# Optimization experiments

Measured on AMD Instinct MI355X. Metric: run time of the kernel, lower is better.

The kernel has to match this reference:

```python
import jax, jax.numpy as jnp
import numpy as np

N, E = 50000, 800000
S, V, RBF_DIM = 128, 16, 16
RBF_DMAX = 20.0
MSG_NORM = 10.0
EPS = 1e-8
DVH_M = V + 1            # message GVP: dim_vectors_in = V + 1 (edge direction appended), dim_h = max(17,16) = 17
FIN_M = S + RBF_DIM      # message GVP scalar input = node scalars + rbf(dist)
DVH_U = 2 * V            # update GVP: dim_vectors_in = 2V (node + aggregated), dim_h = 32
FIN_U = 2 * S


def _rbf(D):
    # [E] -> [E, RBF_DIM], matches torch _rbf with D_min=0, D_max=20, D_count=16
    D_mu = jnp.linspace(0.0, RBF_DMAX, RBF_DIM)
    D_sigma = RBF_DMAX / RBF_DIM
    return jnp.exp(-(((D[:, None] - D_mu[None, :]) / D_sigma) ** 2))


def _gvp(s, v, Wh, Wu, Wf, bf, Wg, bg):
    # s: [n, F_in], v: [n, V_in, 3]; faithful to GVP.forward with sigmoid vector gating
    Vh = jnp.einsum('nvc,vh->nhc', v, Wh)          # [n, H, 3]
    Vu = jnp.einsum('nhc,ho->noc', Vh, Wu)         # [n, V_out, 3]
    sh = jnp.sqrt(jnp.clip(jnp.sum(Vh * Vh, -1), EPS))  # _norm_no_nan
    feats_out = jax.nn.silu(jnp.concatenate([s, sh], -1) @ Wf + bf)
    gate = jax.nn.sigmoid(feats_out @ Wg + bg)[..., None]
    return feats_out, gate * Vu


def _gvp_layernorm(s, v, gamma, beta):
    mu = jnp.mean(s, -1, keepdims=True)
    var = jnp.mean((s - mu) ** 2, -1, keepdims=True)
    s_out = (s - mu) / jnp.sqrt(var + 1e-5) * gamma + beta
    vn = jnp.clip(jnp.sum(v * v, -1, keepdims=True), EPS)        # [N, V, 1]
    vn = jnp.sqrt(jnp.mean(vn, -2, keepdims=True) + 1e-5) + 1e-5  # [N, 1, 1]
    return s_out, v / vn


def setup_inputs() -> dict:
    key = jax.random.key(0)
    ks = jax.random.split(key, 14)
    rn = lambda k, shp, sc: (jax.random.normal(k, shp, dtype=jnp.float32) * sc)
    inp = {
        's': rn(ks[0], (N, S), 1.0),
        'v': rn(ks[1], (N, V, 3), 1.0),
        'x': rn(ks[2], (N, 3), 5.0),
        # message GVP params
        'Wh_m': rn(ks[3], (DVH_M, DVH_M), 1.0 / np.sqrt(DVH_M)),
        'Wu_m': rn(ks[4], (DVH_M, V), 1.0 / np.sqrt(DVH_M)),
        'Wf_m': rn(ks[5], (DVH_M + FIN_M, S), 1.0 / np.sqrt(DVH_M + FIN_M)),
        'bf_m': jnp.zeros((S,), jnp.float32),
        'Wg_m': rn(ks[6], (S, V), 1.0 / np.sqrt(S)),
        'bg_m': jnp.zeros((V,), jnp.float32),
        # update GVP params
        'Wh_u': rn(ks[7], (DVH_U, DVH_U), 1.0 / np.sqrt(DVH_U)),
        'Wu_u': rn(ks[8], (DVH_U, V), 1.0 / np.sqrt(DVH_U)),
        'Wf_u': rn(ks[9], (DVH_U + FIN_U, S), 1.0 / np.sqrt(DVH_U + FIN_U)),
        'bf_u': jnp.zeros((S,), jnp.float32),
        'Wg_u': rn(ks[10], (S, V), 1.0 / np.sqrt(S)),
        'bg_u': jnp.zeros((V,), jnp.float32),
        # layernorm
        'ln_g': jnp.ones((S,), jnp.float32),
        'ln_b': jnp.zeros((S,), jnp.float32),
        'edge_index': jax.random.randint(ks[11], (2, E), 0, N),
    }
    return inp


def reference(s, v, x, Wh_m, Wu_m, Wf_m, bf_m, Wg_m, bg_m,
              Wh_u, Wu_u, Wf_u, bf_u, Wg_u, bg_u, ln_g, ln_b, edge_index):
    src, dst = edge_index[0], edge_index[1]
    # gather + geometric edge features
    dx = x[dst] - x[src]                                   # [E, 3]
    dist = jnp.sqrt(jnp.clip(jnp.sum(dx * dx, -1), EPS))    # [E]
    unit = dx / dist[:, None]
    v_in = jnp.concatenate([v[src], unit[:, None, :]], 1)   # [E, V+1, 3]
    s_in = jnp.concatenate([s[src], _rbf(dist)], -1)        # [E, S+RBF]
    # message GVP
    ms, mv = _gvp(s_in, v_in, Wh_m, Wu_m, Wf_m, bf_m, Wg_m, bg_m)
    # scatter-reduce + message norm
    agg_s = jax.ops.segment_sum(ms, dst, num_segments=N) / MSG_NORM   # [N, S]
    agg_v = jax.ops.segment_sum(mv, dst, num_segments=N) / MSG_NORM   # [N, V, 3]
    # update GVP on concatenated node + aggregated messages
    us, uv = _gvp(jnp.concatenate([s, agg_s], -1), jnp.concatenate([v, agg_v], 1),
                  Wh_u, Wu_u, Wf_u, bf_u, Wg_u, bg_u)
    # residual + GVPLayerNorm
    return _gvp_layernorm(s + us, v + uv, ln_g, ln_b)
```

## Files before the change

### kernel.cpp

```cpp
#include <hip/hip_runtime.h>
#include <hip/hip_bf16.h>
#include <math.h>

#define N_NODES 50000
#define E_EDGES 800000
#define S_DIM 128
#define V_DIM 16
#define HM 17
#define KM 161
#define HU 32
#define KU 288

#define EB 32
#define LDA 164
#define NB 32
#define LDA2 292

__device__ __forceinline__ float bf2f(unsigned short u) {
    union { unsigned int i; float f; } w; w.i = ((unsigned int)u) << 16; return w.f;
}
__device__ __forceinline__ unsigned short f2bf(float f) {
    union { float f; unsigned int i; } w; w.f = f;
    unsigned int x = w.i;
    x += 0x7fff + ((x >> 16) & 1);
    return (unsigned short)(x >> 16);
}
__device__ __forceinline__ float silu_f(float x) { return x / (1.f + __expf(-x)); }
__device__ __forceinline__ float sigm_f(float x) { return 1.f / (1.f + __expf(-x)); }
__device__ __forceinline__ float ldf(const void* p, int i, int m) {
    if (m) return ((const float*)p)[i];
    return bf2f(((const unsigned short*)p)[i]);
}

__global__ void detect_kernel(const unsigned short* __restrict__ s_us,
                              int* __restrict__ flag) {
    int t = threadIdx.x;
    int huge = 0;
    for (int k = 0; k < 16; ++k) {
        unsigned short u = s_us[2 * (t + 64 * k)];
        int e = (u >> 7) & 0xFF;
        if (e > 140) huge = 1;
    }
    if (huge) atomicOr(flag, 1);
}

__global__ void hist_kernel(const int* __restrict__ ei, int* __restrict__ cnt) {
    int i = blockIdx.x * 256 + threadIdx.x;
    if (i < E_EDGES) atomicAdd(&cnt[ei[E_EDGES + i]], 1);
}

__global__ void scan_kernel(int* __restrict__ cnt) {
    __shared__ int buf[1024];
    __shared__ int base_s;
    const int t = threadIdx.x;
    if (t == 0) base_s = 0;
    __syncthreads();
    for (int c0 = 0; c0 < N_NODES; c0 += 1024) {
        int i = c0 + t;
        int v = (i < N_NODES) ? cnt[i] : 0;
        buf[t] = v;
        __syncthreads();
        for (int off = 1; off < 1024; off <<= 1) {
            int tmp = (t >= off) ? buf[t - off] : 0;
            __syncthreads();
            buf[t] += tmp;
            __syncthreads();
        }
        int base = base_s;
        if (i < N_NODES) cnt[i] = base + buf[t] - v;
        __syncthreads();
        if (t == 0) base_s = base + buf[1023];
        __syncthreads();
    }
}

__global__ void scatter_kernel(const int* __restrict__ ei,
                               int* __restrict__ cnt,
                               int* __restrict__ perm) {
    int i = blockIdx.x * 256 + threadIdx.x;
    if (i < E_EDGES) {
        int d = ei[E_EDGES + i];
        int p = atomicAdd(&cnt[d], 1);
        perm[p] = i;
    }
}

__global__ __launch_bounds__(256, 4) void edge_kernel(
    const void* sP, const void* vP, const void* xP,
    const void* WhP, const void* WuP, const void* WfP,
    const void* bfP, const void* WgP, const void* bgP,
    const int* __restrict__ ei,
    const int* __restrict__ perm,
    const int* __restrict__ flagp,
    float* __restrict__ agg_s,
    float* __restrict__ agg_v)
{
    __shared__ float A[EB * LDA];
    __shared__ float Bs[2048];
    __shared__ float WhWu[HM * 16];
    __shared__ float gates[EB * 16];
    __shared__ int srcb[EB], dstb[EB];

    const int t = threadIdx.x;
    const int e0 = blockIdx.x * EB;
    const int m = flagp[0];

    if (t < EB) {
        int eid = perm[e0 + t];
        srcb[t] = ei[eid];
        dstb[t] = ei[E_EDGES + eid];
    }
    if (m) {
        const float* Wh = (const float*)WhP;
        const float* Wu = (const float*)WuP;
        for (int i = t; i < HM * HM; i += 256) gates[i] = Wh[i];
        for (int i = t; i < HM * 16; i += 256) Bs[1664 + i] = Wu[i];
    } else {
        const unsigned short* Wh = (const unsigned short*)WhP;
        const unsigned short* Wu = (const unsigned short*)WuP;
        for (int i = t; i < HM * HM; i += 256) gates[i] = bf2f(Wh[i]);
        for (int i = t; i < HM * 16; i += 256) Bs[1664 + i] = bf2f(Wu[i]);
    }
    __syncthreads();

    for (int idx = t; idx < HM * 16; idx += 256) {
        int vv = idx / 16, o = idx % 16;
        float acc = 0.f;
        for (int h = 0; h < HM; ++h)
            acc += gates[vv * HM + h] * Bs[1664 + h * 16 + o];
        WhWu[idx] = acc;
    }
    {
        int tj = t & 31, te = t >> 5;
        if (m) {
            const float* sF = (const float*)sP;
            for (int r = 0; r < 4; ++r) {
                int e = te + 8 * r;
                float4 u = *(const float4*)(sF + (size_t)srcb[e] * S_DIM + tj * 4);
                float* a = &A[e * LDA + tj * 4];
                a[0] = u.x; a[1] = u.y; a[2] = u.z; a[3] = u.w;
            }
        } else {
            const unsigned short* sU = (const unsigned short*)sP;
            for (int r = 0; r < 4; ++r) {
                int e = te + 8 * r;
                ushort4 u = *(const ushort4*)(sU + (size_t)srcb[e] * S_DIM + tj * 4);
                float* a = &A[e * LDA + tj * 4];
                a[0] = bf2f(u.x); a[1] = bf2f(u.y); a[2] = bf2f(u.z); a[3] = bf2f(u.w);
            }
        }
    }
    if (t < 128) {
        int e = t >> 2, q = t & 3;
        int src = srcb[e];
        float* vin = &Bs[e * 52 + q * 12];
        if (m) {
            const float* vp = (const float*)vP + (size_t)src * 48 + q * 12;
            for (int i = 0; i < 3; ++i) {
                float4 u = *(const float4*)(vp + i * 4);
                vin[i * 4 + 0] = u.x; vin[i * 4 + 1] = u.y;
                vin[i * 4 + 2] = u.z; vin[i * 4 + 3] = u.w;
            }
        } else {
            const unsigned short* vp = (const unsigned short*)vP + (size_t)src * 48 + q * 12;
            for (int i = 0; i < 3; ++i) {
                ushort4 u = *(const ushort4*)(vp + i * 4);
                vin[i * 4 + 0] = bf2f(u.x); vin[i * 4 + 1] = bf2f(u.y);
                vin[i * 4 + 2] = bf2f(u.z); vin[i * 4 + 3] = bf2f(u.w);
            }
        }
        if (q == 0) {
            int dst = dstb[e];
            float dxc[3]; float d2 = 0.f;
            for (int c = 0; c < 3; ++c) {
                float xs = ldf(xP, src * 3 + c, m);
                float xd = ldf(xP, dst * 3 + c, m);
                dxc[c] = xd - xs; d2 += dxc[c] * dxc[c];
            }
            float dist = sqrtf(fmaxf(d2, 1e-8f));
            float inv = 1.f / dist;
            for (int c = 0; c < 3; ++c) Bs[e * 52 + 48 + c] = dxc[c] * inv;
            for (int k = 0; k < 16; ++k) {
                float mu = (20.f / 15.f) * (float)k;
                float z = (dist - mu) * (1.f / 1.25f);
                A[e * LDA + 128 + k] = __expf(-z * z);
            }
        }
    }
    __syncthreads();

    for (int idx = t; idx < EB * HM; idx += 256) {
        int e = idx / HM, h = idx % HM;
        const float* vin = &Bs[e * 52];
        float vh0 = 0.f, vh1 = 0.f, vh2 = 0.f;
        for (int vv = 0; vv < HM; ++vv) {
            float w = gates[vv * HM + h];
            vh0 += vin[vv * 3 + 0] * w;
            vh1 += vin[vv * 3 + 1] * w;
            vh2 += vin[vv * 3 + 2] * w;
        }
        A[e * LDA + 144 + h] = sqrtf(fmaxf(vh0 * vh0 + vh1 * vh1 + vh2 * vh2, 1e-8f));
    }
    float vureg[6];
    for (int r = 0; r < 6; ++r) {
        int idx = t + 256 * r;
        int e = idx / 48, oc = idx % 48, o = oc / 3, c = oc % 3;
        const float* vin = &Bs[e * 52];
        float acc = 0.f;
        for (int vv = 0; vv < HM; ++vv)
            acc += vin[vv * 3 + c] * WhWu[vv * 16 + o];
        vureg[r] = acc;
    }
    __syncthreads();

    const int tj = t & 15, te = t >> 4;
    const int eb = te * 2;
    float acc[2][8];
    #pragma unroll
    for (int i = 0; i < 2; ++i)
        #pragma unroll
        for (int j = 0; j < 8; ++j) acc[i][j] = 0.f;

    for (int kk = 0; kk < KM; kk += 16) {
        int kmax = min(16, KM - kk);
        if (m) {
            const float* WfF = (const float*)WfP;
            for (int idx = t; idx < kmax * 32; idx += 256) {
                int kt = idx >> 5, col4 = (idx & 31) * 4;
                float4 u = *(const float4*)(WfF + (size_t)(kk + kt) * 128 + col4);
                float* b = &Bs[kt * 128 + col4];
                b[0] = u.x; b[1] = u.y; b[2] = u.z; b[3] = u.w;
            }
        } else {
            const unsigned short* WfU = (const unsigned short*)WfP;
            for (int idx = t; idx < kmax * 32; idx += 256) {
                int kt = idx >> 5, col4 = (idx & 31) * 4;
                ushort4 u = *(const ushort4*)(WfU + (size_t)(kk + kt) * 128 + col4);
                float* b = &Bs[kt * 128 + col4];
                b[0] = bf2f(u.x); b[1] = bf2f(u.y); b[2] = bf2f(u.z); b[3] = bf2f(u.w);
            }
        }
        __syncthreads();
        for (int kt = 0; kt < kmax; ++kt) {
            float a0 = A[(eb + 0) * LDA + kk + kt];
            float a1 = A[(eb + 1) * LDA + kk + kt];
            const float* brow = &Bs[kt * 128 + tj];
            #pragma unroll
            for (int jj = 0; jj < 8; ++jj) {
                float b = brow[16 * jj];
                acc[0][jj] += a0 * b; acc[1][jj] += a1 * b;
            }
        }
        __syncthreads();
    }
    float breg[8];
    #pragma unroll
    for (int jj = 0; jj < 8; ++jj) breg[jj] = ldf(bfP, tj + 16 * jj, m);
    #pragma unroll
    for (int i = 0; i < 2; ++i) {
        float* aout = &A[(eb + i) * LDA];
        #pragma unroll
        for (int jj = 0; jj < 8; ++jj)
            aout[tj + 16 * jj] = silu_f(acc[i][jj] + breg[jj]);
    }
    __syncthreads();
    if (m) {
        const float* Wg = (const float*)WgP;
        for (int i = t; i < 2048; i += 256) Bs[i] = Wg[i];
    } else {
        const unsigned short* Wg = (const unsigned short*)WgP;
        for (int i = t; i < 2048; i += 256) Bs[i] = bf2f(Wg[i]);
    }
    __syncthreads();
    for (int r = 0; r < 2; ++r) {
        int idx = t + 256 * r;
        int e = idx / 16, o = idx % 16;
        const float* fe = &A[e * LDA];
        float g = ldf(bgP, o, m);
        for (int j = 0; j < S_DIM; ++j)
            g += fe[j] * Bs[j * 16 + o];
        gates[idx] = sigm_f(g);
    }
    __syncthreads();
    for (int r = 0; r < 6; ++r) {
        int idx = t + 256 * r;
        int e = idx / 48, oc = idx % 48, o = oc / 3;
        (void)oc;
        Bs[idx] = vureg[r] * gates[e * 16 + o];
    }
    __syncthreads();
    if (t < 176) {
        float run = 0.f;
        int cur = dstb[0];
        if (t < 128) {
            const int col = t;
            for (int e = 0; e < EB; ++e) {
                int d = dstb[e];
                if (d != cur) {
                    atomicAdd(&agg_s[(size_t)cur * S_DIM + col], run);
                    run = 0.f; cur = d;
                }
                run += A[e * LDA + col];
            }
            atomicAdd(&agg_s[(size_t)cur * S_DIM + col], run);
        } else {
            const int oc = t - 128;
            for (int e = 0; e < EB; ++e) {
                int d = dstb[e];
                if (d != cur) {
                    atomicAdd(&agg_v[(size_t)cur * 48 + oc], run);
                    run = 0.f; cur = d;
                }
                run += Bs[e * 48 + oc];
            }
            atomicAdd(&agg_v[(size_t)cur * 48 + oc], run);
        }
    }
}

__global__ __launch_bounds__(256) void node_kernel(
    const void* sP, const void* vP,
    const void* WhP, const void* WuP, const void* WfP,
    const void* bfP, const void* WgP, const void* bgP,
    const void* lngP, const void* lnbP,
    const int* __restrict__ flagp,
    const float* __restrict__ agg_s,
    const float* __restrict__ agg_v,
    void* outP)
{
    __shared__ float A2[NB * LDA2];
    __shared__ float Bs2[4096];
    __shared__ float WhWu2[HU * 16];
    __shared__ float gates2[NB * 16];
    __shared__ float WhS[HU * HU];
    __shared__ float mu_s[NB], rstd_s[NB], vn_s[NB];

    const int t = threadIdx.x;
    const int n0 = blockIdx.x * NB;
    const int m = flagp[0];

    if (m) {
        const float* Wh = (const float*)WhP;
        const float* Wu = (const float*)WuP;
        for (int i = t; i < HU * HU; i += 256) WhS[i] = Wh[i];
        for (int i = t; i < HU * 16; i += 256) gates2[i] = Wu[i];
    } else {
        const unsigned short* Wh = (const unsigned short*)WhP;
        const unsigned short* Wu = (const unsigned short*)WuP;
        for (int i = t; i < HU * HU; i += 256) WhS[i] = bf2f(Wh[i]);
        for (int i = t; i < HU * 16; i += 256) gates2[i] = bf2f(Wu[i]);
    }
    if (m) {
        const float* sF = (const float*)sP;
        for (int idx = t; idx < NB * 32; idx += 256) {
            int ni = idx >> 5, col4 = (idx & 31) * 4;
            int n = n0 + ni;
            float* a = &A2[ni * LDA2 + col4];
            if (n < N_NODES) {
                float4 u = *(const float4*)(sF + (size_t)n * 128 + col4);
                a[0] = u.x; a[1] = u.y; a[2] = u.z; a[3] = u.w;
            } else { a[0] = a[1] = a[2] = a[3] = 0.f; }
        }
    } else {
        const unsigned short* sU = (const unsigned short*)sP;
        for (int idx = t; idx < NB * 32; idx += 256) {
            int ni = idx >> 5, col4 = (idx & 31) * 4;
            int n = n0 + ni;
            float* a = &A2[ni * LDA2 + col4];
            if (n < N_NODES) {
                ushort4 u = *(const ushort4*)(sU + (size_t)n * 128 + col4);
                a[0] = bf2f(u.x); a[1] = bf2f(u.y); a[2] = bf2f(u.z); a[3] = bf2f(u.w);
            } else { a[0] = a[1] = a[2] = a[3] = 0.f; }
        }
    }
    for (int idx = t; idx < NB * 32; idx += 256) {
        int ni = idx >> 5, col4 = (idx & 31) * 4;
        int n = n0 + ni;
        float* a = &A2[ni * LDA2 + 128 + col4];
        if (n < N_NODES) {
            float4 u = *(const float4*)(agg_s + (size_t)n * 128 + col4);
            a[0] = u.x * 0.1f; a[1] = u.y * 0.1f; a[2] = u.z * 0.1f; a[3] = u.w * 0.1f;
        } else { a[0] = a[1] = a[2] = a[3] = 0.f; }
    }
    for (int idx = t; idx < NB * 96; idx += 256) {
        int ni = idx / 96, vc = idx % 96;
        int n = n0 + ni;
        float val = 0.f;
        if (n < N_NODES)
            val = (vc < 48) ? ldf(vP, n * 48 + vc, m)
                            : agg_v[(size_t)n * 48 + (vc - 48)] * 0.1f;
        Bs2[ni * 100 + vc] = val;
    }
    __syncthreads();
    for (int idx = t; idx < HU * 16; idx += 256) {
        int vv = idx / 16, o = idx % 16;
        float acc = 0.f;
        for (int h = 0; h < HU; ++h)
            acc += WhS[vv * HU + h] * gates2[h * 16 + o];
        WhWu2[idx] = acc;
// ... 69 lines not shown
        #pragma unroll
        for (int jj = 0; jj < 8; ++jj)
            aout[tj + 16 * jj] = silu_f(acc[i][jj] + breg[jj]);
    }
    __syncthreads();
    if (m) {
        const float* Wg = (const float*)WgP;
        for (int i = t; i < 2048; i += 256) Bs2[i] = Wg[i];
    } else {
        const unsigned short* Wg = (const unsigned short*)WgP;
        for (int i = t; i < 2048; i += 256) Bs2[i] = bf2f(Wg[i]);
    }
    __syncthreads();
    for (int r = 0; r < 2; ++r) {
        int idx = t + 256 * r;
        int ni = idx / 16, o = idx % 16;
        const float* fe = &A2[ni * LDA2 + 128];
        float g = ldf(bgP, o, m);
        for (int j = 0; j < 128; ++j)
            g += fe[j] * Bs2[j * 16 + o];
        gates2[idx] = sigm_f(g);
    }
    __syncthreads();
    for (int r = 0; r < 6; ++r) {
        int idx = t + 256 * r;
        int ni = idx / 48, oc = idx % 48, o = oc / 3;
        int n = n0 + ni;
        float vres = 0.f;
        if (n < N_NODES)
            vres = ldf(vP, n * 48 + oc, m) + vureg[r] * gates2[ni * 16 + o];
        Bs2[ni * 48 + oc] = vres;
    }
    __syncthreads();
    if (t < NB) {
        const float* arow = &A2[t * LDA2];
        float sum = 0.f, sumsq = 0.f;
        for (int j = 0; j < 128; ++j) {
            float xr = arow[j] + arow[128 + j];
            sum += xr; sumsq += xr * xr;
        }
        float mu = sum * (1.f / 128.f);
        float var = sumsq * (1.f / 128.f) - mu * mu;
        mu_s[t] = mu;
        rstd_s[t] = rsqrtf(fmaxf(var, 0.f) + 1e-5f);
        const float* vr = &Bs2[t * 48];
        float accv = 0.f;
        for (int o = 0; o < 16; ++o) {
            float mm = vr[o*3]*vr[o*3] + vr[o*3+1]*vr[o*3+1] + vr[o*3+2]*vr[o*3+2];
            accv += fmaxf(mm, 1e-8f);
        }
        vn_s[t] = sqrtf(accv * (1.f / 16.f) + 1e-5f) + 1e-5f;
    }
    __syncthreads();
    float* outF = (float*)outP;
    unsigned short* outU = (unsigned short*)outP;
    for (int idx = t; idx < NB * 128; idx += 256) {
        int ni = idx >> 7, j = idx & 127;
        int n = n0 + ni;
        if (n < N_NODES) {
            float xr = A2[ni * LDA2 + j] + A2[ni * LDA2 + 128 + j];
            float o = (xr - mu_s[ni]) * rstd_s[ni] * ldf(lngP, j, m) + ldf(lnbP, j, m);
            if (m) outF[(size_t)n * 128 + j] = o;
            else   outU[(size_t)n * 128 + j] = f2bf(o);
        }
    }
    for (int idx = t; idx < NB * 48; idx += 256) {
        int ni = idx / 48, oc = idx % 48;
        int n = n0 + ni;
        if (n < N_NODES) {
            float o = Bs2[ni * 48 + oc] / vn_s[ni];
            if (m) outF[(size_t)N_NODES * 128 + (size_t)n * 48 + oc] = o;
            else   outU[(size_t)N_NODES * 128 + (size_t)n * 48 + oc] = f2bf(o);
        }
    }
}

extern "C" void kernel_launch(void* const* d_in, const int* in_sizes, int n_in,
                              void* d_out, int out_size, void* d_ws, size_t ws_size,
                              hipStream_t stream) {
    const int* ei = (const int*)d_in[17];

    int* flag = (int*)d_ws;
    int* cnt = (int*)((char*)d_ws + 64);
    float* agg_s = (float*)((char*)d_ws + 64 + 200000);
    float* agg_v = agg_s + (size_t)N_NODES * 128;
    int* perm = (int*)(agg_v + (size_t)N_NODES * 48);

    hipMemsetAsync(d_ws, 0,
                   64 + 200000 + (size_t)N_NODES * (128 + 48) * sizeof(float),
                   stream);

    detect_kernel<<<1, 64, 0, stream>>>((const unsigned short*)d_in[0], flag);

    hist_kernel<<<(E_EDGES + 255) / 256, 256, 0, stream>>>(ei, cnt);
    scan_kernel<<<1, 1024, 0, stream>>>(cnt);
    scatter_kernel<<<(E_EDGES + 255) / 256, 256, 0, stream>>>(ei, cnt, perm);

    edge_kernel<<<E_EDGES / EB, 256, 0, stream>>>(
        d_in[0], d_in[1], d_in[2], d_in[3], d_in[4], d_in[5],
        d_in[6], d_in[7], d_in[8], ei, perm, flag, agg_s, agg_v);
    node_kernel<<<(N_NODES + NB - 1) / NB, 256, 0, stream>>>(
        d_in[0], d_in[1], d_in[9], d_in[10], d_in[11], d_in[12],
        d_in[13], d_in[14], d_in[15], d_in[16], flag,
        agg_s, agg_v, d_out);
}
```

Baseline: 2.534 ms.

## Precompute per-node linear terms of message GVP before edge gather

Adds a prep kernel that computes, once per source node, s·Wf[:128], the partial vector projection v·Wh and its Wu projection. The edge kernel then gathers these precomputed rows and adds only the edge-dependent terms (rbf, unit vector, vector norms) through a 33-row matmul. This moves the 128-wide scalar matmul from 800k edges to 50k nodes, at the cost of an extra kernel, extra workspace and gathering 128+51+48 floats per edge instead of 128+48 raw inputs.

```diff
diff --git a/kernel.cpp b/kernel.cpp
--- a/kernel.cpp
+++ b/kernel.cpp
@@ -12,9 +12,9 @@
 #define KU 288
 
 #define EB 32
-#define LDA 164
 #define NB 32
 #define LDA2 292
+#define LDF 132
 
 __device__ __forceinline__ float bf2f(unsigned short u) {
     union { unsigned int i; float f; } w; w.i = ((unsigned int)u) << 16; return w.f;
@@ -85,166 +85,113 @@
     }
 }
 
-__global__ __launch_bounds__(256, 4) void edge_kernel(
-    const void* sP, const void* vP, const void* xP,
+__global__ __launch_bounds__(256, 4) void prep_kernel(
+    const void* sP, const void* vP,
     const void* WhP, const void* WuP, const void* WfP,
-    const void* bfP, const void* WgP, const void* bgP,
-    const int* __restrict__ ei,
-    const int* __restrict__ perm,
     const int* __restrict__ flagp,
-    float* __restrict__ agg_s,
-    float* __restrict__ agg_v)
+    float* __restrict__ Pg, float* __restrict__ Qg, float* __restrict__ Rg,
+    float* __restrict__ whwu16)
 {
-    __shared__ float A[EB * LDA];
-    __shared__ float Bs[2048];
-    __shared__ float WhWu[HM * 16];
-    __shared__ float gates[EB * 16];
-    __shared__ int srcb[EB], dstb[EB];
+    __shared__ float sA[NB * 132];
+    __shared__ float Wfb[16 * 128];
+    __shared__ float vtile[NB * 48];
+    __shared__ float WhS[HM * HM];
+    __shared__ float WuS[HM * 16];
 
     const int t = threadIdx.x;
-    const int e0 = blockIdx.x * EB;
+    const int n0 = blockIdx.x * NB;
     const int m = flagp[0];
 
-    if (t < EB) {
-        int eid = perm[e0 + t];
-        srcb[t] = ei[eid];
-        dstb[t] = ei[E_EDGES + eid];
-    }
     if (m) {
         const float* Wh = (const float*)WhP;
         const float* Wu = (const float*)WuP;
-        for (int i = t; i < HM * HM; i += 256) gates[i] = Wh[i];
-        for (int i = t; i < HM * 16; i += 256) Bs[1664 + i] = Wu[i];
+        for (int i = t; i < HM * HM; i += 256) WhS[i] = Wh[i];
+        for (int i = t; i < HM * 16; i += 256) WuS[i] = Wu[i];
     } else {
         const unsigned short* Wh = (const unsigned short*)WhP;
         const unsigned short* Wu = (const unsigned short*)WuP;
-        for (int i = t; i < HM * HM; i += 256) gates[i] = bf2f(Wh[i]);
-        for (int i = t; i < HM * 16; i += 256) Bs[1664 + i] = bf2f(Wu[i]);
-    }
-    __syncthreads();
-
-    for (int idx = t; idx < HM * 16; idx += 256) {
-        int vv = idx / 16, o = idx % 16;
-        float acc = 0.f;
-        for (int h = 0; h < HM; ++h)
-            acc += gates[vv * HM + h] * Bs[1664 + h * 16 + o];
-        WhWu[idx] = acc;
-    }
-    {
-        int tj = t & 31, te = t >> 5;
-        if (m) {
-            const float* sF = (const float*)sP;
-            for (int r = 0; r < 4; ++r) {
-                int e = te + 8 * r;
-                float4 u = *(const float4*)(sF + (size_t)srcb[e] * S_DIM + tj * 4);
-                float* a = &A[e * LDA + tj * 4];
+        for (int i = t; i < HM * HM; i += 256) WhS[i] = bf2f(Wh[i]);
+        for (int i = t; i < HM * 16; i += 256) WuS[i] = bf2f(Wu[i]);
+    }
+    if (m) {
+        const float* sF = (const float*)sP;
+        for (int idx = t; idx < NB * 32; idx += 256) {
+            int ni = idx >> 5, col4 = (idx & 31) * 4;
+            int n = n0 + ni;
+            float* a = &sA[ni * 132 + col4];
+            if (n < N_NODES) {
+                float4 u = *(const float4*)(sF + (size_t)n * 128 + col4);
                 a[0] = u.x; a[1] = u.y; a[2] = u.z; a[3] = u.w;
-            }
-        } else {
-            const unsigned short* sU = (const unsigned short*)sP;
-            for (int r = 0; r < 4; ++r) {
-                int e = te + 8 * r;
-                ushort4 u = *(const ushort4*)(sU + (size_t)srcb[e] * S_DIM + tj * 4);
-                float* a = &A[e * LDA + tj * 4];
+            } else { a[0] = a[1] = a[2] = a[3] = 0.f; }
+        }
+    } else {
+        const unsigned short* sU = (const unsigned short*)sP;
+        for (int idx = t; idx < NB * 32; idx += 256) {
+            int ni = idx >> 5, col4 = (idx & 31) * 4;
+            int n = n0 + ni;
+            float* a = &sA[ni * 132 + col4];
+            if (n < N_NODES) {
+                ushort4 u = *(const ushort4*)(sU + (size_t)n * 128 + col4);
                 a[0] = bf2f(u.x); a[1] = bf2f(u.y); a[2] = bf2f(u.z); a[3] = bf2f(u.w);
-            }
-        }
-    }
-    if (t < 128) {
-        int e = t >> 2, q = t & 3;
-        int src = srcb[e];
-        float* vin = &Bs[e * 52 + q * 12];
-        if (m) {
-            const float* vp = (const float*)vP + (size_t)src * 48 + q * 12;
-            for (int i = 0; i < 3; ++i) {
-                float4 u = *(const float4*)(vp + i * 4);
-                vin[i * 4 + 0] = u.x; vin[i * 4 + 1] = u.y;
-                vin[i * 4 + 2] = u.z; vin[i * 4 + 3] = u.w;
-            }
-        } else {
-            const unsigned short* vp = (const unsigned short*)vP + (size_t)src * 48 + q * 12;
-            for (int i = 0; i < 3; ++i) {
-                ushort4 u = *(const ushort4*)(vp + i * 4);
-                vin[i * 4 + 0] = bf2f(u.x); vin[i * 4 + 1] = bf2f(u.y);
-                vin[i * 4 + 2] = bf2f(u.z); vin[i * 4 + 3] = bf2f(u.w);
-            }
-        }
-        if (q == 0) {
-            int dst = dstb[e];
-            float dxc[3]; float d2 = 0.f;
-            for (int c = 0; c < 3; ++c) {
-                float xs = ldf(xP, src * 3 + c, m);
-                float xd = ldf(xP, dst * 3 + c, m);
-                dxc[c] = xd - xs; d2 += dxc[c] * dxc[c];
-            }
-            float dist = sqrtf(fmaxf(d2, 1e-8f));
-            float inv = 1.f / dist;
-            for (int c = 0; c < 3; ++c) Bs[e * 52 + 48 + c] = dxc[c] * inv;
-            for (int k = 0; k < 16; ++k) {
-                float mu = (20.f / 15.f) * (float)k;
-                float z = (dist - mu) * (1.f / 1.25f);
-                A[e * LDA + 128 + k] = __expf(-z * z);
-            }
-        }
-    }
-    __syncthreads();
-
-    for (int idx = t; idx < EB * HM; idx += 256) {
-        int e = idx / HM, h = idx % HM;
-        const float* vin = &Bs[e * 52];
-        float vh0 = 0.f, vh1 = 0.f, vh2 = 0.f;
-        for (int vv = 0; vv < HM; ++vv) {
-            float w = gates[vv * HM + h];
-            vh0 += vin[vv * 3 + 0] * w;
-            vh1 += vin[vv * 3 + 1] * w;
-            vh2 += vin[vv * 3 + 2] * w;
-        }
-        A[e * LDA + 144 + h] = sqrtf(fmaxf(vh0 * vh0 + vh1 * vh1 + vh2 * vh2, 1e-8f));
-    }
-    float vureg[6];
-    for (int r = 0; r < 6; ++r) {
-        int idx = t + 256 * r;
-        int e = idx / 48, oc = idx % 48, o = oc / 3, c = oc % 3;
-        const float* vin = &Bs[e * 52];
-        float acc = 0.f;
-        for (int vv = 0; vv < HM; ++vv)
-            acc += vin[vv * 3 + c] * WhWu[vv * 16 + o];
-        vureg[r] = acc;
-    }
-    __syncthreads();
-
-    const int tj = t & 15, te = t >> 4;
-    const int eb = te * 2;
+            } else { a[0] = a[1] = a[2] = a[3] = 0.f; }
+        }
+    }
+    if (m) {
+        const float* vF = (const float*)vP;
+        for (int idx = t; idx < NB * 12; idx += 256) {
+            int ni = idx / 12, c4 = (idx % 12) * 4;
+            int n = n0 + ni;
+            float* a = &vtile[ni * 48 + c4];
+            if (n < N_NODES) {
+                float4 u = *(const float4*)(vF + (size_t)n * 48 + c4);
+                a[0] = u.x; a[1] = u.y; a[2] = u.z; a[3] = u.w;
+            } else { a[0] = a[1] = a[2] = a[3] = 0.f; }
+        }
+    } else {
+        const unsigned short* vU = (const unsigned short*)vP;
+        for (int idx = t; idx < NB * 12; idx += 256) {
+            int ni = idx / 12, c4 = (idx % 12) * 4;
+            int n = n0 + ni;
+            float* a = &vtile[ni * 48 + c4];
+            if (n < N_NODES) {
+                ushort4 u = *(const ushort4*)(vU + (size_t)n * 48 + c4);
+                a[0] = bf2f(u.x); a[1] = bf2f(u.y); a[2] = bf2f(u.z); a[3] = bf2f(u.w);
+            } else { a[0] = a[1] = a[2] = a[3] = 0.f; }
+        }
+    }
+    __syncthreads();
+
+    const int tj = t & 15, tn = t >> 4;
+    const int nb = tn * 2;
     float acc[2][8];
     #pragma unroll
     for (int i = 0; i < 2; ++i)
         #pragma unroll
         for (int j = 0; j < 8; ++j) acc[i][j] = 0.f;
 
-    for (int kk = 0; kk < KM; kk += 16) {
-        int kmax = min(16, KM - kk);
+    for (int kk = 0; kk < 128; kk += 16) {
         if (m) {
             const float* WfF = (const float*)WfP;
-            for (int idx = t; idx < kmax * 32; idx += 256) {
+            for (int idx = t; idx < 512; idx += 256) {
                 int kt = idx >> 5, col4 = (idx & 31) * 4;
                 float4 u = *(const float4*)(WfF + (size_t)(kk + kt) * 128 + col4);
-                float* b = &Bs[kt * 128 + col4];
+                float* b = &Wfb[kt * 128 + col4];
                 b[0] = u.x; b[1] = u.y; b[2] = u.z; b[3] = u.w;
             }
         } else {
             const unsigned short* WfU = (const unsigned short*)WfP;
-            for (int idx = t; idx < kmax * 32; idx += 256) {
+            for (int idx = t; idx < 512; idx += 256) {
                 int kt = idx >> 5, col4 = (idx & 31) * 4;
                 ushort4 u = *(const ushort4*)(WfU + (size_t)(kk + kt) * 128 + col4);
-                float* b = &Bs[kt * 128 + col4];
+                float* b = &Wfb[kt * 128 + col4];
                 b[0] = bf2f(u.x); b[1] = bf2f(u.y); b[2] = bf2f(u.z); b[3] = bf2f(u.w);
             }
         }
         __syncthreads();
-        for (int kt = 0; kt < kmax; ++kt) {
-            float a0 = A[(eb + 0) * LDA + kk + kt];
-            float a1 = A[(eb + 1) * LDA + kk + kt];
-            const float* brow = &Bs[kt * 128 + tj];
+        for (int kt = 0; kt < 16; ++kt) {
+            float a0 = sA[(nb + 0) * 132 + kk + kt];
+            float a1 = sA[(nb + 1) * 132 + kk + kt];
+            const float* brow = &Wfb[kt * 128 + tj];
             #pragma unroll
             for (int jj = 0; jj < 8; ++jj) {
                 float b = brow[16 * jj];
@@ -253,40 +200,183 @@
         }
         __syncthreads();
     }
-    float breg[8];
-    #pragma unroll
-    for (int jj = 0; jj < 8; ++jj) breg[jj] = ldf(bfP, tj + 16 * jj, m);
     #pragma unroll
     for (int i = 0; i < 2; ++i) {
-        float* aout = &A[(eb + i) * LDA];
+        int n = n0 + nb + i;
+        if (n < N_NODES) {
+            #pragma unroll
+            for (int jj = 0; jj < 8; ++jj)
+                Pg[(size_t)n * 128 + tj + 16 * jj] = acc[i][jj];
+        }
+    }
+
+    float* qtile = Wfb;
+    for (int idx = t; idx < NB * 51; idx += 256) {
+        int ni = idx / 51, rem = idx % 51;
+        int h = rem / 3, c = rem % 3;
+        float q = 0.f;
+        for (int vv = 0; vv < 16; ++vv)
+            q += vtile[ni * 48 + vv * 3 + c] * WhS[vv * HM + h];
+        qtile[idx] = q;
+        int n = n0 + ni;
+        if (n < N_NODES) Qg[(size_t)n * 51 + rem] = q;
+    }
+    __syncthreads();
+    for (int idx = t; idx < NB * 48; idx += 256) {
+        int ni = idx / 48, oc = idx % 48;
+        int o = oc / 3, c = oc % 3;
+        float r = 0.f;
+        for (int h = 0; h < HM; ++h)
+            r += qtile[ni * 51 + h * 3 + c] * WuS[h * 16 + o];
+        int n = n0 + ni;
+        if (n < N_NODES) Rg[(size_t)n * 48 + oc] = r;
+    }
+    if (blockIdx.x == 0 && t < 16) {
+        float a = 0.f;
+        for (int h = 0; h < HM; ++h)
+            a += WhS[16 * HM + h] * WuS[h * 16 + t];
+        whwu16[t] = a;
+    }
+}
+
+__global__ __launch_bounds__(256, 4) void edge_kernel(
+    const void* xP, const void* WhP, const void* WfP,
+    const void* bfP, const void* WgP, const void* bgP,
+    const int* __restrict__ ei,
+    const int* __restrict__ perm,
+    const int* __restrict__ flagp,
+    const float* __restrict__ Pg,
+    const float* __restrict__ Qg,
+    const float* __restrict__ Rg,
+    const float* __restrict__ whwu16,
+    float* __restrict__ agg_s,
+    float* __restrict__ agg_v)
+{
+    __shared__ float Wb[33 * 128];
+    __shared__ float A33[EB * 33];
+    __shared__ float Xb[2048];
+    __shared__ float gates[EB * 16];
+    __shared__ float unitb[EB * 3];
+    __shared__ float whs[16];
+    __shared__ int srcb[EB], dstb[EB];
+
+    const int t = threadIdx.x;
+    const int e0 = blockIdx.x * EB;
+    const int m = flagp[0];
+
+    if (t < EB) {
+        int eid = perm[e0 + t];
+        srcb[t] = ei[eid];
+        dstb[t] = ei[E_EDGES + eid];
+    }
+    if (t < 16) whs[t] = whwu16[t];
+    if (m) {
+        const float* Wf = (const float*)WfP + 128 * 128;
+        for (int idx = t; idx < 33 * 32; idx += 256) {
+            int kt = idx >> 5, col4 = (idx & 31) * 4;
+            float4 u = *(const float4*)(Wf + kt * 128 + col4);
+            float* b = &Wb[kt * 128 + col4];
+            b[0] = u.x; b[1] = u.y; b[2] = u.z; b[3] = u.w;
+        }
+    } else {
+        const unsigned short* Wf = (const unsigned short*)WfP + 128 * 128;
+        for (int idx = t; idx < 33 * 32; idx += 256) {
+            int kt = idx >> 5, col4 = (idx & 31) * 4;
+            ushort4 u = *(const ushort4*)(Wf + kt * 128 + col4);
+            float* b = &Wb[kt * 128 + col4];
+            b[0] = bf2f(u.x); b[1] = bf2f(u.y); b[2] = bf2f(u.z); b[3] = bf2f(u.w);
+        }
+    }
+    __syncthreads();
+
+    const int tj = t & 15, te = t >> 4;
+    const int eb = te * 2;
+    float acc[2][8];
+    #pragma unroll
+    for (int i = 0; i < 2; ++i) {
+        const float* prow = Pg + (size_t)srcb[eb + i] * 128 + tj;
         #pragma unroll
-        for (int jj = 0; jj < 8; ++jj)
-            aout[tj + 16 * jj] = silu_f(acc[i][jj] + breg[jj]);
-    }
-    __syncthreads();
+        for (int jj = 0; jj < 8; ++jj) acc[i][jj] = prow[16 * jj];
+    }
+
+    if (t < EB) {
+        int src = srcb[t], dst = dstb[t];
+        float dxc[3]; float d2 = 0.f;
+        for (int c = 0; c < 3; ++c) {
+            float xs = ldf(xP, src * 3 + c, m);
+            float xd = ldf(xP, dst * 3 + c, m);
+            dxc[c] = xd - xs; d2 += dxc[c] * dxc[c];
+        }
+        float dist = sqrtf(fmaxf(d2, 1e-8f));
+        float inv = 1.f / dist;
+        for (int c = 0; c < 3; ++c) unitb[t * 3 + c] = dxc[c] * inv;
+        for (int k = 0; k < 16; ++k) {
+            float mu = (20.f / 15.f) * (float)k;
+            float z = (dist - mu) * (1.f / 1.25f);
+            A33[t * 33 + k] = __expf(-z * z);
+        }
+    }
+    __syncthreads();
+    for (int idx = t; idx < EB * HM; idx += 256) {
+        int e = idx / HM, h = idx % HM;
+        float w = ldf(WhP, 16 * HM + h, m);
+        const float* q = Qg + (size_t)srcb[e] * 51 + h * 3;
+        float v0 = q[0] + unitb[e * 3 + 0] * w;
+        float v1 = q[1] + unitb[e * 3 + 1] * w;
+        float v2 = q[2] + unitb[e * 3 + 2] * w;
+        A33[e * 33 + 16 + h] = sqrtf(fmaxf(v0 * v0 + v1 * v1 + v2 * v2, 1e-8f));
+    }
+    __syncthreads();
+
+    for (int kt = 0; kt < 33; ++kt) {
+        float a0 = A33[(eb + 0) * 33 + kt];
+        float a1 = A33[(eb + 1) * 33 + kt];
+        const float* brow = &Wb[kt * 128 + tj];
+        #pragma unroll
+        for (int jj = 0; jj < 8; ++jj) {
+            float b = brow[16 * jj];
+            acc[0][jj] += a0 * b; acc[1][jj] += a1 * b;
+        }
+    }
     if (m) {
         const float* Wg = (const float*)WgP;
-        for (int i = t; i < 2048; i += 256) Bs[i] = Wg[i];
+        for (int i = t; i < 2048; i += 256) Xb[i] = Wg[i];
     } else {
         const unsigned short* Wg = (const unsigned short*)WgP;
-        for (int i = t; i < 2048; i += 256) Bs[i] = bf2f(Wg[i]);
-    }
-    __syncthreads();
-    for (int r = 0; r < 2; ++r) {
-        int idx = t + 256 * r;
-        int e = idx / 16, o = idx % 16;
-        const float* fe = &A[e * LDA];
-        float g = ldf(bgP, o, m);
-        for (int j = 0; j < S_DIM; ++j)
-            g += fe[j] * Bs[j * 16 + o];
-        gates[idx] = sigm_f(g);
+        for (int i = t; i < 2048; i += 256) Xb[i] = bf2f(Wg[i]);
+    }
+    __syncthreads();
+    {
+        float breg[8];
+        #pragma unroll
+        for (int jj = 0; jj < 8; ++jj) breg[jj] = ldf(bfP, tj + 16 * jj, m);
+        #pragma unroll
+        for (int i = 0; i < 2; ++i) {
+            float* aout = &Wb[(eb + i) * LDF];
+            #pragma unroll
+            for (int jj = 0; jj < 8; ++jj)
+                aout[tj + 16 * jj] = silu_f(acc[i][jj] + breg[jj]);
+        }
+    }
+    __syncthreads();
+    {
+        int e = t >> 3, o0 = (t & 7) * 2;
+        float g0 = ldf(bgP, o0, m), g1 = ldf(bgP, o0 + 1, m);
+        const float* fe = &Wb[e * LDF];
+        for (int j = 0; j < S_DIM; ++j) {
+            float f = fe[j];
+            g0 += f * Xb[j * 16 + o0];
+            g1 += f * Xb[j * 16 + o0 + 1];
+        }
+        gates[e * 16 + o0]     = sigm_f(g0);
+        gates[e * 16 + o0 + 1] = sigm_f(g1);
     }
     __syncthreads();
     for (int r = 0; r < 6; ++r) {
         int idx = t + 256 * r;
-        int e = idx / 48, oc = idx % 48, o = oc / 3;
-        (void)oc;
-        Bs[idx] = vureg[r] * gates[e * 16 + o];
+        int e = idx / 48, oc = idx % 48, o = oc / 3, c = oc % 3;
+        float vu = Rg[(size_t)srcb[e] * 48 + oc] + unitb[e * 3 + c] * whs[o];
+        Xb[idx] = vu * gates[e * 16 + o];
     }
     __syncthreads();
     if (t < 176) {
@@ -300,7 +390,7 @@
                     atomicAdd(&agg_s[(size_t)cur * S_DIM + col], run);
                     run = 0.f; cur = d;
                 }
-                run += A[e * LDA + col];
+                run += Wb[e * LDF + col];
             }
             atomicAdd(&agg_s[(size_t)cur * S_DIM + col], run);
         } else {
@@ -311,7 +401,7 @@
                     atomicAdd(&agg_v[(size_t)cur * 48 + oc], run);
                     run = 0.f; cur = d;
                 }
-                run += Bs[e * 48 + oc];
+                run += Xb[e * 48 + oc];
             }
             atomicAdd(&agg_v[(size_t)cur * 48 + oc], run);
         }
@@ -550,12 +640,16 @@
 
     int* flag = (int*)d_ws;
     int* cnt = (int*)((char*)d_ws + 64);
-    float* agg_s = (float*)((char*)d_ws + 64 + 200000);
+    float* whwu16 = (float*)((char*)d_ws + 64 + 200000);
+    float* agg_s = (float*)((char*)d_ws + 64 + 200000 + 64);
     float* agg_v = agg_s + (size_t)N_NODES * 128;
     int* perm = (int*)(agg_v + (size_t)N_NODES * 48);
+    float* Pg = (float*)(perm + E_EDGES);
+    float* Qg = Pg + (size_t)N_NODES * 128;
+    float* Rg = Qg + (size_t)N_NODES * 51;
 
     hipMemsetAsync(d_ws, 0,
-                   64 + 200000 + (size_t)N_NODES * (128 + 48) * sizeof(float),
+                   64 + 200000 + 64 + (size_t)N_NODES * (128 + 48) * sizeof(float),
                    stream);
 
     detect_kernel<<<1, 64, 0, stream>>>((const unsigned short*)d_in[0], flag);
@@ -564,9 +658,12 @@
     scan_kernel<<<1, 1024, 0, stream>>>(cnt);
     scatter_kernel<<<(E_EDGES + 255) / 256, 256, 0, stream>>>(ei, cnt, perm);
 
+    prep_kernel<<<(N_NODES + NB - 1) / NB, 256, 0, stream>>>(
+        d_in[0], d_in[1], d_in[3], d_in[4], d_in[5], flag, Pg, Qg, Rg, whwu16);
+
     edge_kernel<<<E_EDGES / EB, 256, 0, stream>>>(
-        d_in[0], d_in[1], d_in[2], d_in[3], d_in[4], d_in[5],
-        d_in[6], d_in[7], d_in[8], ei, perm, flag, agg_s, agg_v);
+        d_in[2], d_in[3], d_in[5], d_in[6], d_in[7], d_in[8],
+        ei, perm, flag, Pg, Qg, Rg, whwu16, agg_s, agg_v);
     node_kernel<<<(N_NODES + NB - 1) / NB, 256, 0, stream>>>(
         d_in[0], d_in[1], d_in[9], d_in[10], d_in[11], d_in[12],
         d_in[13], d_in[14], d_in[15], d_in[16], flag,
```

After: 4.269 ms. +68.5%, slower.

## Assign each block a fixed set of destination nodes and aggregate in shared memory

Applied to the files above, without the earlier changes.

The edge kernel now owns 8 destination nodes per block. It uses the CSR offsets left in cnt after the scatter pass and walks that node range's edges in tiles of 32, accumulating messages in shared memory. Each block then writes agg_s/agg_v directly, so there are no global atomics and the large memset of the aggregation buffers goes away. The scatter pass stores source indices directly rather than a permutation. The cost is load imbalance, since per-block edge counts vary and partial tiles waste work. The per-edge destination lookup is a linear search, and the accumulation loop is serial per column.

```diff
diff --git a/kernel.cpp b/kernel.cpp
--- a/kernel.cpp
+++ b/kernel.cpp
@@ -12,6 +12,7 @@
 #define KU 288
 
 #define EB 32
+#define NPB 8
 #define LDA 164
 #define NB 32
 #define LDA2 292
@@ -76,12 +77,12 @@
 
 __global__ void scatter_kernel(const int* __restrict__ ei,
                                int* __restrict__ cnt,
-                               int* __restrict__ perm) {
+                               int* __restrict__ src_sorted) {
     int i = blockIdx.x * 256 + threadIdx.x;
     if (i < E_EDGES) {
         int d = ei[E_EDGES + i];
         int p = atomicAdd(&cnt[d], 1);
-        perm[p] = i;
+        src_sorted[p] = ei[i];
     }
 }
 
@@ -89,232 +90,258 @@
     const void* sP, const void* vP, const void* xP,
     const void* WhP, const void* WuP, const void* WfP,
     const void* bfP, const void* WgP, const void* bgP,
-    const int* __restrict__ ei,
-    const int* __restrict__ perm,
+    const int* __restrict__ cnt,
+    const int* __restrict__ src_sorted,
     const int* __restrict__ flagp,
     float* __restrict__ agg_s,
     float* __restrict__ agg_v)
 {
     __shared__ float A[EB * LDA];
     __shared__ float Bs[2048];
+    __shared__ float WhS[HM * HM];
     __shared__ float WhWu[HM * 16];
     __shared__ float gates[EB * 16];
-    __shared__ int srcb[EB], dstb[EB];
+    __shared__ float aggs_ls[NPB * 128];
+    __shared__ float aggv_ls[NPB * 48];
+    __shared__ int srcb[EB], dstb[EB], dloc[EB];
+    __shared__ int rp_s[NPB + 1];
 
     const int t = threadIdx.x;
-    const int e0 = blockIdx.x * EB;
+    const int n0 = blockIdx.x * NPB;
     const int m = flagp[0];
 
-    if (t < EB) {
-        int eid = perm[e0 + t];
-        srcb[t] = ei[eid];
-        dstb[t] = ei[E_EDGES + eid];
+    if (t <= NPB) {
+        int n = n0 + t;
+        if (n > N_NODES) n = N_NODES;
+        rp_s[t] = (n == 0) ? 0 : cnt[n - 1];
     }
     if (m) {
         const float* Wh = (const float*)WhP;
         const float* Wu = (const float*)WuP;
-        for (int i = t; i < HM * HM; i += 256) gates[i] = Wh[i];
+        for (int i = t; i < HM * HM; i += 256) WhS[i] = Wh[i];
         for (int i = t; i < HM * 16; i += 256) Bs[1664 + i] = Wu[i];
     } else {
         const unsigned short* Wh = (const unsigned short*)WhP;
         const unsigned short* Wu = (const unsigned short*)WuP;
-        for (int i = t; i < HM * HM; i += 256) gates[i] = bf2f(Wh[i]);
+        for (int i = t; i < HM * HM; i += 256) WhS[i] = bf2f(Wh[i]);
         for (int i = t; i < HM * 16; i += 256) Bs[1664 + i] = bf2f(Wu[i]);
     }
+    for (int i = t; i < NPB * 128; i += 256) aggs_ls[i] = 0.f;
+    for (int i = t; i < NPB * 48; i += 256) aggv_ls[i] = 0.f;
     __syncthreads();
 
     for (int idx = t; idx < HM * 16; idx += 256) {
         int vv = idx / 16, o = idx % 16;
         float acc = 0.f;
         for (int h = 0; h < HM; ++h)
-            acc += gates[vv * HM + h] * Bs[1664 + h * 16 + o];
+            acc += WhS[vv * HM + h] * Bs[1664 + h * 16 + o];
         WhWu[idx] = acc;
     }
-    {
-        int tj = t & 31, te = t >> 5;
-        if (m) {
-            const float* sF = (const float*)sP;
-            for (int r = 0; r < 4; ++r) {
-                int e = te + 8 * r;
-                float4 u = *(const float4*)(sF + (size_t)srcb[e] * S_DIM + tj * 4);
-                float* a = &A[e * LDA + tj * 4];
-                a[0] = u.x; a[1] = u.y; a[2] = u.z; a[3] = u.w;
-            }
-        } else {
-            const unsigned short* sU = (const unsigned short*)sP;
-            for (int r = 0; r < 4; ++r) {
-                int e = te + 8 * r;
-                ushort4 u = *(const ushort4*)(sU + (size_t)srcb[e] * S_DIM + tj * 4);
-                float* a = &A[e * LDA + tj * 4];
-                a[0] = bf2f(u.x); a[1] = bf2f(u.y); a[2] = bf2f(u.z); a[3] = bf2f(u.w);
-            }
-        }
-    }
-    if (t < 128) {
-        int e = t >> 2, q = t & 3;
-        int src = srcb[e];
-        float* vin = &Bs[e * 52 + q * 12];
-        if (m) {
-            const float* vp = (const float*)vP + (size_t)src * 48 + q * 12;
-            for (int i = 0; i < 3; ++i) {
-                float4 u = *(const float4*)(vp + i * 4);
-                vin[i * 4 + 0] = u.x; vin[i * 4 + 1] = u.y;
-                vin[i * 4 + 2] = u.z; vin[i * 4 + 3] = u.w;
-            }
-        } else {
-            const unsigned short* vp = (const unsigned short*)vP + (size_t)src * 48 + q * 12;
-            for (int i = 0; i < 3; ++i) {
-                ushort4 u = *(const ushort4*)(vp + i * 4);
-                vin[i * 4 + 0] = bf2f(u.x); vin[i * 4 + 1] = bf2f(u.y);
-                vin[i * 4 + 2] = bf2f(u.z); vin[i * 4 + 3] = bf2f(u.w);
-            }
-        }
-        if (q == 0) {
-            int dst = dstb[e];
-            float dxc[3]; float d2 = 0.f;
-            for (int c = 0; c < 3; ++c) {
-                float xs = ldf(xP, src * 3 + c, m);
-                float xd = ldf(xP, dst * 3 + c, m);
-                dxc[c] = xd - xs; d2 += dxc[c] * dxc[c];
-            }
-            float dist = sqrtf(fmaxf(d2, 1e-8f));
-            float inv = 1.f / dist;
-            for (int c = 0; c < 3; ++c) Bs[e * 52 + 48 + c] = dxc[c] * inv;
-            for (int k = 0; k < 16; ++k) {
-                float mu = (20.f / 15.f) * (float)k;
-                float z = (dist - mu) * (1.f / 1.25f);
-                A[e * LDA + 128 + k] = __expf(-z * z);
-            }
-        }
-    }
-    __syncthreads();
-
-    for (int idx = t; idx < EB * HM; idx += 256) {
-        int e = idx / HM, h = idx % HM;
-        const float* vin = &Bs[e * 52];
-        float vh0 = 0.f, vh1 = 0.f, vh2 = 0.f;
-        for (int vv = 0; vv < HM; ++vv) {
-            float w = gates[vv * HM + h];
-            vh0 += vin[vv * 3 + 0] * w;
-            vh1 += vin[vv * 3 + 1] * w;
-            vh2 += vin[vv * 3 + 2] * w;
-        }
-        A[e * LDA + 144 + h] = sqrtf(fmaxf(vh0 * vh0 + vh1 * vh1 + vh2 * vh2, 1e-8f));
-    }
-    float vureg[6];
-    for (int r = 0; r < 6; ++r) {
-        int idx = t + 256 * r;
-        int e = idx / 48, oc = idx % 48, o = oc / 3, c = oc % 3;
-        const float* vin = &Bs[e * 52];
-        float acc = 0.f;
-        for (int vv = 0; vv < HM; ++vv)
-            acc += vin[vv * 3 + c] * WhWu[vv * 16 + o];
-        vureg[r] = acc;
-    }
-    __syncthreads();
+
+    const int eBase = rp_s[0];
+    const int eTot = rp_s[NPB] - rp_s[0];
+    const int ntiles = (eTot + EB - 1) / EB;
 
     const int tj = t & 15, te = t >> 4;
     const int eb = te * 2;
-    float acc[2][8];
-    #pragma unroll
-    for (int i = 0; i < 2; ++i)
-        #pragma unroll
-        for (int j = 0; j < 8; ++j) acc[i][j] = 0.f;
-
-    for (int kk = 0; kk < KM; kk += 16) {
-        int kmax = min(16, KM - kk);
-        if (m) {
-            const float* WfF = (const float*)WfP;
-            for (int idx = t; idx < kmax * 32; idx += 256) {
-                int kt = idx >> 5, col4 = (idx & 31) * 4;
-                float4 u = *(const float4*)(WfF + (size_t)(kk + kt) * 128 + col4);
-                float* b = &Bs[kt * 128 + col4];
-                b[0] = u.x; b[1] = u.y; b[2] = u.z; b[3] = u.w;
-            }
-        } else {
-            const unsigned short* WfU = (const unsigned short*)WfP;
-            for (int idx = t; idx < kmax * 32; idx += 256) {
-                int kt = idx >> 5, col4 = (idx & 31) * 4;
-                ushort4 u = *(const ushort4*)(WfU + (size_t)(kk + kt) * 128 + col4);
-                float* b = &Bs[kt * 128 + col4];
-                b[0] = bf2f(u.x); b[1] = bf2f(u.y); b[2] = bf2f(u.z); b[3] = bf2f(u.w);
-            }
-        }
-        __syncthreads();
-        for (int kt = 0; kt < kmax; ++kt) {
-            float a0 = A[(eb + 0) * LDA + kk + kt];
-            float a1 = A[(eb + 1) * LDA + kk + kt];
-            const float* brow = &Bs[kt * 128 + tj];
-            #pragma unroll
-            for (int jj = 0; jj < 8; ++jj) {
-                float b = brow[16 * jj];
-                acc[0][jj] += a0 * b; acc[1][jj] += a1 * b;
-            }
-        }
-        __syncthreads();
-    }
     float breg[8];
     #pragma unroll
     for (int jj = 0; jj < 8; ++jj) breg[jj] = ldf(bfP, tj + 16 * jj, m);
-    #pragma unroll
-    for (int i = 0; i < 2; ++i) {
-        float* aout = &A[(eb + i) * LDA];
+
+    __syncthreads();
+
+    for (int tile = 0; tile < ntiles; ++tile) {
+        const int ecnt = min(EB, eTot - tile * EB);
+
+        if (t < EB) {
+            if (t < ecnt) {
+                int p = eBase + tile * EB + t;
+                srcb[t] = src_sorted[p];
+                int dl = 0;
+                while (dl < NPB - 1 && rp_s[dl + 1] <= p) ++dl;
+                dloc[t] = dl;
+                dstb[t] = n0 + dl;
+            } else {
+                srcb[t] = 0; dloc[t] = 0; dstb[t] = 0;
+            }
+        }
+        __syncthreads();
+
+        {
+            int cj = t & 31, ce = t >> 5;
+            if (m) {
+                const float* sF = (const float*)sP;
+                for (int r = 0; r < 4; ++r) {
+                    int e = ce + 8 * r;
+                    float4 u = *(const float4*)(sF + (size_t)srcb[e] * S_DIM + cj * 4);
+                    float* a = &A[e * LDA + cj * 4];
+                    a[0] = u.x; a[1] = u.y; a[2] = u.z; a[3] = u.w;
+                }
+            } else {
+                const unsigned short* sU = (const unsigned short*)sP;
+                for (int r = 0; r < 4; ++r) {
+                    int e = ce + 8 * r;
+                    ushort4 u = *(const ushort4*)(sU + (size_t)srcb[e] * S_DIM + cj * 4);
+                    float* a = &A[e * LDA + cj * 4];
+                    a[0] = bf2f(u.x); a[1] = bf2f(u.y); a[2] = bf2f(u.z); a[3] = bf2f(u.w);
+                }
+            }
+        }
+        if (t < 128) {
+            int e = t >> 2, q = t & 3;
+            int src = srcb[e];
+            float* vin = &Bs[e * 52 + q * 12];
+            if (m) {
+                const float* vp = (const float*)vP + (size_t)src * 48 + q * 12;
+                for (int i = 0; i < 3; ++i) {
+                    float4 u = *(const float4*)(vp + i * 4);
+                    vin[i * 4 + 0] = u.x; vin[i * 4 + 1] = u.y;
+                    vin[i * 4 + 2] = u.z; vin[i * 4 + 3] = u.w;
+                }
+            } else {
+                const unsigned short* vp = (const unsigned short*)vP + (size_t)src * 48 + q * 12;
+                for (int i = 0; i < 3; ++i) {
+                    ushort4 u = *(const ushort4*)(vp + i * 4);
+                    vin[i * 4 + 0] = bf2f(u.x); vin[i * 4 + 1] = bf2f(u.y);
+                    vin[i * 4 + 2] = bf2f(u.z); vin[i * 4 + 3] = bf2f(u.w);
+                }
+            }
+            if (q == 0) {
+                int dst = dstb[e];
+                float dxc[3]; float d2 = 0.f;
+                for (int c = 0; c < 3; ++c) {
+                    float xs = ldf(xP, src * 3 + c, m);
+                    float xd = ldf(xP, dst * 3 + c, m);
+                    dxc[c] = xd - xs; d2 += dxc[c] * dxc[c];
+                }
+                float dist = sqrtf(fmaxf(d2, 1e-8f));
+                float inv = 1.f / dist;
+                for (int c = 0; c < 3; ++c) Bs[e * 52 + 48 + c] = dxc[c] * inv;
+                for (int k = 0; k < 16; ++k) {
+                    float mu = (20.f / 15.f) * (float)k;
+                    float z = (dist - mu) * (1.f / 1.25f);
+                    A[e * LDA + 128 + k] = __expf(-z * z);
+                }
+            }
+        }
+        __syncthreads();
+
+        for (int idx = t; idx < EB * HM; idx += 256) {
+            int e = idx / HM, h = idx % HM;
+            const float* vin = &Bs[e * 52];
+            float vh0 = 0.f, vh1 = 0.f, vh2 = 0.f;
+            for (int vv = 0; vv < HM; ++vv) {
+                float w = WhS[vv * HM + h];
+                vh0 += vin[vv * 3 + 0] * w;
+                vh1 += vin[vv * 3 + 1] * w;
+                vh2 += vin[vv * 3 + 2] * w;
+            }
+            A[e * LDA + 144 + h] = sqrtf(fmaxf(vh0 * vh0 + vh1 * vh1 + vh2 * vh2, 1e-8f));
+        }
+        float vureg[6];
+        for (int r = 0; r < 6; ++r) {
+            int idx = t + 256 * r;
+            int e = idx / 48, oc = idx % 48, o = oc / 3, c = oc % 3;
+            const float* vin = &Bs[e * 52];
+            float acc = 0.f;
+            for (int vv = 0; vv < HM; ++vv)
+                acc += vin[vv * 3 + c] * WhWu[vv * 16 + o];
+            vureg[r] = acc;
+        }
+        __syncthreads();
+
+        float acc[2][8];
         #pragma unroll
-        for (int jj = 0; jj < 8; ++jj)
-            aout[tj + 16 * jj] = silu_f(acc[i][jj] + breg[jj]);
-    }
-    __syncthreads();
-    if (m) {
-        const float* Wg = (const float*)WgP;
-        for (int i = t; i < 2048; i += 256) Bs[i] = Wg[i];
-    } else {
-        const unsigned short* Wg = (const unsigned short*)WgP;
-        for (int i = t; i < 2048; i += 256) Bs[i] = bf2f(Wg[i]);
-    }
-    __syncthreads();
-    for (int r = 0; r < 2; ++r) {
-        int idx = t + 256 * r;
-        int e = idx / 16, o = idx % 16;
-        const float* fe = &A[e * LDA];
-        float g = ldf(bgP, o, m);
-        for (int j = 0; j < S_DIM; ++j)
-            g += fe[j] * Bs[j * 16 + o];
-        gates[idx] = sigm_f(g);
-    }
-    __syncthreads();
-    for (int r = 0; r < 6; ++r) {
-        int idx = t + 256 * r;
-        int e = idx / 48, oc = idx % 48, o = oc / 3;
-        (void)oc;
-        Bs[idx] = vureg[r] * gates[e * 16 + o];
-    }
-    __syncthreads();
-    if (t < 176) {
-        float run = 0.f;
-        int cur = dstb[0];
-        if (t < 128) {
-            const int col = t;
-            for (int e = 0; e < EB; ++e) {
-                int d = dstb[e];
-                if (d != cur) {
-                    atomicAdd(&agg_s[(size_t)cur * S_DIM + col], run);
-                    run = 0.f; cur = d;
-                }
-                run += A[e * LDA + col];
-            }
-            atomicAdd(&agg_s[(size_t)cur * S_DIM + col], run);
+        for (int i = 0; i < 2; ++i)
+            #pragma unroll
+            for (int j = 0; j < 8; ++j) acc[i][j] = 0.f;
+
+        for (int kk = 0; kk < KM; kk += 16) {
+            int kmax = min(16, KM - kk);
+            if (m) {
+                const float* WfF = (const float*)WfP;
+                for (int idx = t; idx < kmax * 32; idx += 256) {
+                    int kt = idx >> 5, col4 = (idx & 31) * 4;
+                    float4 u = *(const float4*)(WfF + (size_t)(kk + kt) * 128 + col4);
+                    float* b = &Bs[kt * 128 + col4];
+                    b[0] = u.x; b[1] = u.y; b[2] = u.z; b[3] = u.w;
+                }
+            } else {
+                const unsigned short* WfU = (const unsigned short*)WfP;
+                for (int idx = t; idx < kmax * 32; idx += 256) {
+                    int kt = idx >> 5, col4 = (idx & 31) * 4;
+                    ushort4 u = *(const ushort4*)(WfU + (size_t)(kk + kt) * 128 + col4);
+                    float* b = &Bs[kt * 128 + col4];
+                    b[0] = bf2f(u.x); b[1] = bf2f(u.y); b[2] = bf2f(u.z); b[3] = bf2f(u.w);
+                }
+            }
+            __syncthreads();
+            for (int kt = 0; kt < kmax; ++kt) {
+                float a0 = A[(eb + 0) * LDA + kk + kt];
+                float a1 = A[(eb + 1) * LDA + kk + kt];
+                const float* brow = &Bs[kt * 128 + tj];
+                #pragma unroll
+                for (int jj = 0; jj < 8; ++jj) {
+                    float b = brow[16 * jj];
+                    acc[0][jj] += a0 * b; acc[1][jj] += a1 * b;
+                }
+            }
+            __syncthreads();
+        }
+        #pragma unroll
+        for (int i = 0; i < 2; ++i) {
+            float* aout = &A[(eb + i) * LDA];
+            #pragma unroll
+            for (int jj = 0; jj < 8; ++jj)
+                aout[tj + 16 * jj] = silu_f(acc[i][jj] + breg[jj]);
+        }
+        __syncthreads();
+        if (m) {
+            const float* Wg = (const float*)WgP;
+            for (int i = t; i < 2048; i += 256) Bs[i] = Wg[i];
         } else {
-            const int oc = t - 128;
-            for (int e = 0; e < EB; ++e) {
-                int d = dstb[e];
-                if (d != cur) {
-                    atomicAdd(&agg_v[(size_t)cur * 48 + oc], run);
-                    run = 0.f; cur = d;
-                }
-                run += Bs[e * 48 + oc];
-            }
-            atomicAdd(&agg_v[(size_t)cur * 48 + oc], run);
-        }
+            const unsigned short* Wg = (const unsigned short*)WgP;
+            for (int i = t; i < 2048; i += 256) Bs[i] = bf2f(Wg[i]);
+        }
+        __syncthreads();
+        for (int r = 0; r < 2; ++r) {
+            int idx = t + 256 * r;
+            int e = idx / 16, o = idx % 16;
+            const float* fe = &A[e * LDA];
+            float g = ldf(bgP, o, m);
+            for (int j = 0; j < S_DIM; ++j)
+                g += fe[j] * Bs[j * 16 + o];
+            gates[idx] = sigm_f(g);
+        }
+        __syncthreads();
+        for (int r = 0; r < 6; ++r) {
+            int idx = t + 256 * r;
+            int e = idx / 48, oc = idx % 48, o = oc / 3;
+            (void)oc;
+            Bs[idx] = vureg[r] * gates[e * 16 + o];
+        }
+        __syncthreads();
+        if (t < 176) {
+            if (t < 128) {
+                const int col = t;
+                for (int e = 0; e < ecnt; ++e)
+                    aggs_ls[dloc[e] * 128 + col] += A[e * LDA + col];
+            } else {
+                const int oc = t - 128;
+                for (int e = 0; e < ecnt; ++e)
+                    aggv_ls[dloc[e] * 48 + oc] += Bs[e * 48 + oc];
+            }
+        }
+        __syncthreads();
+    }
+
+    for (int idx = t; idx < NPB * 128; idx += 256) {
+        int n = n0 + (idx >> 7);
+        if (n < N_NODES) agg_s[(size_t)n * 128 + (idx & 127)] = aggs_ls[idx];
+    }
+    for (int idx = t; idx < NPB * 48; idx += 256) {
+        int n = n0 + idx / 48;
+        if (n < N_NODES) agg_v[(size_t)n * 48 + idx % 48] = aggv_ls[idx];
     }
 }
 
@@ -550,23 +577,21 @@
 
     int* flag = (int*)d_ws;
     int* cnt = (int*)((char*)d_ws + 64);
-    float* agg_s = (float*)((char*)d_ws + 64 + 200000);
+    int* src_sorted = (int*)((char*)d_ws + 64 + 200000);
+    float* agg_s = (float*)(src_sorted + E_EDGES);
     float* agg_v = agg_s + (size_t)N_NODES * 128;
-    int* perm = (int*)(agg_v + (size_t)N_NODES * 48);
-
-    hipMemsetAsync(d_ws, 0,
-                   64 + 200000 + (size_t)N_NODES * (128 + 48) * sizeof(float),
-                   stream);
+
+    hipMemsetAsync(d_ws, 0, 64 + 200000, stream);
 
     detect_kernel<<<1, 64, 0, stream>>>((const unsigned short*)d_in[0], flag);
 
     hist_kernel<<<(E_EDGES + 255) / 256, 256, 0, stream>>>(ei, cnt);
     scan_kernel<<<1, 1024, 0, stream>>>(cnt);
-    scatter_kernel<<<(E_EDGES + 255) / 256, 256, 0, stream>>>(ei, cnt, perm);
-
-    edge_kernel<<<E_EDGES / EB, 256, 0, stream>>>(
+    scatter_kernel<<<(E_EDGES + 255) / 256, 256, 0, stream>>>(ei, cnt, src_sorted);
+
+    edge_kernel<<<(N_NODES + NPB - 1) / NPB, 256, 0, stream>>>(
         d_in[0], d_in[1], d_in[2], d_in[3], d_in[4], d_in[5],
-        d_in[6], d_in[7], d_in[8], ei, perm, flag, agg_s, agg_v);
+        d_in[6], d_in[7], d_in[8], cnt, src_sorted, flag, agg_s, agg_v);
     node_kernel<<<(N_NODES + NB - 1) / NB, 256, 0, stream>>>(
         d_in[0], d_in[1], d_in[9], d_in[10], d_in[11], d_in[12],
         d_in[13], d_in[14], d_in[15], d_in[16], flag,
```

Result: slower. 3.817 ms (+50.7%).
